# Performance work log

Hardware: AMD Instinct MI355X
Metric: run time of the kernel (lower is better)

The kernel has to match this reference:

```python
import jax, jax.numpy as jnp
import numpy as np

SCALE = 0.02  # init scale for weight matrices


def setup_inputs() -> dict:
    B, M, H = 2048, 64, 1024
    key = jax.random.key(0)
    ks = jax.random.split(key, 10)
    inp = {
        "pose_embed": jax.random.normal(ks[0], (B, H), jnp.float32),
        "query_embed": jax.random.normal(ks[1], (B, H), jnp.float32),
        "h": jax.random.normal(ks[2], (B, H), jnp.float32),
        "c": jax.random.normal(ks[3], (B, H), jnp.float32),
        "memory": jax.random.normal(ks[4], (B, M, H), jnp.float32),
        "W_ih": jax.random.normal(ks[5], (4 * H, H), jnp.float32) * SCALE,
        "W_hh": jax.random.normal(ks[6], (4 * H, H), jnp.float32) * SCALE,
        "b_ih": jnp.zeros((4 * H,), jnp.float32),
        "b_hh": jnp.zeros((4 * H,), jnp.float32),
        "Wq": jax.random.normal(ks[7], (H, H), jnp.float32) * SCALE,
        "bq": jnp.zeros((H,), jnp.float32),
        "Wk": jax.random.normal(ks[8], (H, H), jnp.float32) * SCALE,
        "bk": jnp.zeros((H,), jnp.float32),
        "Wv": jax.random.normal(ks[9], (H, H), jnp.float32) * SCALE,
        "bv": jnp.zeros((H,), jnp.float32),
    }
    return inp


def reference(pose_embed, query_embed, h, c, memory,
              W_ih, W_hh, b_ih, b_hh, Wq, bq, Wk, bk, Wv, bv):
    H = pose_embed.shape[-1]
    # --- LSTMCell step (torch gate order: i, f, g, o) ---
    gates = pose_embed @ W_ih.T + b_ih + h @ W_hh.T + b_hh  # [B, 4H]
    i_g, f_g, g_g, o_g = jnp.split(gates, 4, axis=-1)
    c_new = jax.nn.sigmoid(f_g) * c + jax.nn.sigmoid(i_g) * jnp.tanh(g_g)
    h_new = jax.nn.sigmoid(o_g) * jnp.tanh(c_new)
    # --- FIFO memory update (detach, pop oldest, append new h) ---
    mem = jnp.concatenate(
        [memory[:, 1:], jax.lax.stop_gradient(h_new)[:, None]], axis=1)  # [B, M, H]
    # --- single-query attention over memory ---
    Q = query_embed @ Wq.T + bq                       # [B, H]
    K = mem @ Wk.T + bk                               # [B, M, H]
    V = mem @ Wv.T + bv                               # [B, M, H]
    scores = jnp.einsum('bh,bmh->bm', Q, K) / jnp.sqrt(jnp.float32(H))
    attn = jax.nn.softmax(scores, axis=-1)            # [B, M]
    attended = jnp.einsum('bm,bmh->bh', attn, V)      # [B, H]
    return attended, h_new, c_new
```

## Files before the change

### kernel.cpp

```cpp
#include <hip/hip_runtime.h>
#include <stdint.h>

typedef __attribute__((ext_vector_type(8))) short short8;
typedef __attribute__((ext_vector_type(4))) float f32x4;
typedef unsigned short u16;

#define SBAR() do { __builtin_amdgcn_sched_barrier(0); \
                    __builtin_amdgcn_s_barrier(); \
                    __builtin_amdgcn_sched_barrier(0); } while (0)

__device__ __forceinline__ u16 f2bf(float f) {
  union { float f; uint32_t u; } v; v.f = f;
  return (u16)((v.u + 0x7FFFu + ((v.u >> 16) & 1u)) >> 16);
}
__device__ __forceinline__ float bf2f(u16 u) {
  union { uint32_t u; float f; } v; v.u = (uint32_t)u << 16; return v.f;
}

__device__ __forceinline__ void gl_lds16(const void* g, void* l) {
  __builtin_amdgcn_global_load_lds(
      (const __attribute__((address_space(1))) void*)g,
      (__attribute__((address_space(3))) void*)l, 16, 0, 0);
}

__global__ __launch_bounds__(256) void gemm_bt(
    const u16* __restrict__ A, const u16* __restrict__ B,
    float* __restrict__ Cf, u16* __restrict__ Cb,
    const float* __restrict__ bias1,
    int M, int N, int K)
{
  __shared__ __align__(16) u16 As[128 * 32];
  __shared__ __align__(16) u16 Bs[128 * 32];
  const int t = threadIdx.x;
  const int lane = t & 63;
  const int w = t >> 6;
  const int wr = w >> 1, wc = w & 1;
  const int m0 = blockIdx.y * 128, n0 = blockIdx.x * 128;
  const int lr = lane & 15;
  const int lk = (lane >> 4) * 8;
  const int srow = t >> 2;
  const int scol = (t & 3) * 8;

  const u16* gA = A + (size_t)(m0 + srow) * K + scol;
  const u16* gB = B + (size_t)(n0 + srow) * K + scol;

  f32x4 acc[4][4] = {};

  for (int k0 = 0; k0 < K; k0 += 32) {
    gl_lds16(gA,                  As + t * 8);
    gl_lds16(gA + (size_t)64 * K, As + 2048 + t * 8);
    gl_lds16(gB,                  Bs + t * 8);
    gl_lds16(gB + (size_t)64 * K, Bs + 2048 + t * 8);
    gA += 32; gB += 32;
    __syncthreads();

    short8 a[4], b[4];
#pragma unroll
    for (int m = 0; m < 4; ++m)
      a[m] = *(const short8*)(As + (wr * 64 + m * 16 + lr) * 32 + lk);
#pragma unroll
    for (int n = 0; n < 4; ++n)
      b[n] = *(const short8*)(Bs + (wc * 64 + n * 16 + lr) * 32 + lk);
#pragma unroll
    for (int m = 0; m < 4; ++m)
#pragma unroll
      for (int n = 0; n < 4; ++n)
        acc[m][n] = __builtin_amdgcn_mfma_f32_16x16x32_bf16(a[m], b[n], acc[m][n], 0, 0, 0);
    __syncthreads();
  }

#pragma unroll
  for (int n = 0; n < 4; ++n) {
    int col = n0 + wc * 64 + n * 16 + lr;
    float bsum = bias1 ? bias1[col] : 0.f;
#pragma unroll
    for (int m = 0; m < 4; ++m) {
#pragma unroll
      for (int r = 0; r < 4; ++r) {
        int row = m0 + wr * 64 + m * 16 + (lane >> 4) * 4 + r;
        float vv = acc[m][n][r] + bsum;
        if (Cf) Cf[(size_t)row * N + col] = vv;
        if (Cb) Cb[(size_t)row * N + col] = f2bf(vv);
      }
    }
  }
}

__global__ __launch_bounds__(512) void gates8_k(
    const u16* __restrict__ Xcat, const u16* __restrict__ Wcat,
    u16* __restrict__ gparts)
{
  __shared__ __align__(16) u16 lds[65536];
  const int t = threadIdx.x;
  const int l = t & 63;
  const int w = t >> 6;
  const int wr = w >> 2, wc = w & 3;
  const int bid = blockIdx.x;
  const int tile = bid >> 1, khalf = bid & 1;
  const int m0 = (tile >> 4) * 256;
  const int n0 = (tile & 15) * 256;
  const int lr = l & 15;
  const int l4 = l >> 4;

  const int sr = l >> 3;
  const int sc = ((l & 7) * 8) ^ ((l >> 5) << 4);

  const u16* Abase = Xcat + (size_t)m0 * 2048 + khalf * 1024 + sc;
  const u16* Bbase = Wcat + (size_t)n0 * 2048 + khalf * 1024 + sc;

  #define STAGE(buf, kt) do {                                                  \
    const int kof_ = (kt) * 64;                                                \
    _Pragma("unroll")                                                          \
    for (int hh = 0; hh < 2; ++hh)                                             \
      _Pragma("unroll")                                                        \
      for (int j = 0; j < 2; ++j) {                                            \
        int row_ = hh * 128 + (w + 8 * j) * 8 + sr;                            \
        char* dA = (char*)lds + (buf) * 65536 + hh * 16384 + (w + 8*j) * 1024 + l * 16; \
        char* dB = dA + 32768;                                                 \
        gl_lds16(Abase + (size_t)row_ * 2048 + kof_, dA);                      \
        gl_lds16(Bbase + (size_t)row_ * 2048 + kof_, dB);                      \
      }                                                                        \
  } while (0)

  auto LDA = [&](int buf, int mf, int s) -> short8 {
    int rr = mf * 16 + lr;
    int cb = (s * 64 + l4 * 16) ^ (((rr >> 2) & 1) << 5);
    return *(const short8*)((const char*)lds + buf * 65536 + wr * 16384 + rr * 128 + cb);
  };
  auto LDB = [&](int buf, int nf, int s) -> short8 {
    int rr = (wc & 1) * 64 + nf * 16 + lr;
    int cb = (s * 64 + l4 * 16) ^ (((rr >> 2) & 1) << 5);
    return *(const short8*)((const char*)lds + buf * 65536 + 32768 + (wc >> 1) * 16384 + rr * 128 + cb);
  };

  f32x4 acc[8][4] = {};

  STAGE(0, 0);
  STAGE(1, 1);
  asm volatile("s_waitcnt vmcnt(8)" ::: "memory");
  SBAR();

  for (int kt = 0; kt < 16; ++kt) {
    const int cur = kt & 1;
    short8 a0[4][2], a1[4][2], b[2][2];
#pragma unroll
    for (int i = 0; i < 4; ++i) { a0[i][0] = LDA(cur, i, 0); a0[i][1] = LDA(cur, i, 1); }
#pragma unroll
    for (int n = 0; n < 2; ++n) { b[n][0] = LDB(cur, n, 0); b[n][1] = LDB(cur, n, 1); }
    __builtin_amdgcn_s_setprio(1);
#pragma unroll
    for (int i = 0; i < 4; ++i)
#pragma unroll
      for (int n = 0; n < 2; ++n)
#pragma unroll
        for (int s = 0; s < 2; ++s)
          acc[i][n] = __builtin_amdgcn_mfma_f32_16x16x32_bf16(a0[i][s], b[n][s], acc[i][n], 0, 0, 0);
    __builtin_amdgcn_s_setprio(0);
#pragma unroll
    for (int i = 0; i < 4; ++i) { a1[i][0] = LDA(cur, 4 + i, 0); a1[i][1] = LDA(cur, 4 + i, 1); }
    __builtin_amdgcn_s_setprio(1);
#pragma unroll
    for (int i = 0; i < 4; ++i)
#pragma unroll
      for (int n = 0; n < 2; ++n)
#pragma unroll
        for (int s = 0; s < 2; ++s)
          acc[4 + i][n] = __builtin_amdgcn_mfma_f32_16x16x32_bf16(a1[i][s], b[n][s], acc[4 + i][n], 0, 0, 0);
    __builtin_amdgcn_s_setprio(0);
#pragma unroll
    for (int n = 0; n < 2; ++n) { b[n][0] = LDB(cur, 2 + n, 0); b[n][1] = LDB(cur, 2 + n, 1); }
    __builtin_amdgcn_s_setprio(1);
#pragma unroll
    for (int i = 0; i < 4; ++i)
#pragma unroll
      for (int n = 0; n < 2; ++n)
#pragma unroll
        for (int s = 0; s < 2; ++s)
          acc[4 + i][2 + n] = __builtin_amdgcn_mfma_f32_16x16x32_bf16(a1[i][s], b[n][s], acc[4 + i][2 + n], 0, 0, 0);
#pragma unroll
    for (int i = 0; i < 4; ++i)
#pragma unroll
      for (int n = 0; n < 2; ++n)
#pragma unroll
        for (int s = 0; s < 2; ++s)
          acc[i][2 + n] = __builtin_amdgcn_mfma_f32_16x16x32_bf16(a0[i][s], b[n][s], acc[i][2 + n], 0, 0, 0);
    __builtin_amdgcn_s_setprio(0);

    SBAR();
    if (kt + 2 < 16) {
      STAGE(cur, kt + 2);
      asm volatile("s_waitcnt vmcnt(8)" ::: "memory");
    } else {
      asm volatile("s_waitcnt vmcnt(0)" ::: "memory");
    }
    SBAR();
  }
  #undef STAGE

  u16* out = gparts + (size_t)khalf * 2048 * 4096;
#pragma unroll
  for (int nf = 0; nf < 4; ++nf) {
    int col = n0 + wc * 64 + nf * 16 + lr;
#pragma unroll
    for (int mf = 0; mf < 8; ++mf)
#pragma unroll
      for (int r = 0; r < 4; ++r) {
        int row = m0 + wr * 128 + mf * 16 + l4 * 4 + r;
        out[(size_t)row * 4096 + col] = f2bf(acc[mf][nf][r]);
      }
  }
}

__global__ __launch_bounds__(256) void attn_k(
    const float* __restrict__ Qk, const float* __restrict__ mem,
    float* __restrict__ attst)
{
  const int t = threadIdx.x;
  const int lane = t & 63;
  const int b = blockIdx.x * 4 + (t >> 6);
  const float* q = Qk + (size_t)b * 1024;
  f32x4 qv[4];
#pragma unroll
  for (int i = 0; i < 4; ++i)
    qv[i] = *(const f32x4*)(q + (i * 64 + lane) * 4);
  const float* mb = mem + (size_t)b * 65536;

  float m_run = -3e38f, l = 0.f;
  f32x4 cx[4] = {};

  for (int qd = 0; qd < 15; ++qd) {
    const float* r0 = mb + (size_t)(1 + qd * 4) * 1024;
    f32x4 rv[4][4];
    float s[4] = {0.f, 0.f, 0.f, 0.f};
#pragma unroll
    for (int rr = 0; rr < 4; ++rr)
#pragma unroll
      for (int i = 0; i < 4; ++i) {
        rv[rr][i] = __builtin_nontemporal_load(
            (const f32x4*)(r0 + rr * 1024 + (i * 64 + lane) * 4));
        s[rr] += rv[rr][i][0] * qv[i][0] + rv[rr][i][1] * qv[i][1] +
                 rv[rr][i][2] * qv[i][2] + rv[rr][i][3] * qv[i][3];
      }
#pragma unroll
    for (int rr = 0; rr < 4; ++rr) {
#pragma unroll
      for (int off = 32; off; off >>= 1) s[rr] += __shfl_xor(s[rr], off);
      s[rr] *= 0.03125f;
    }
#pragma unroll
    for (int rr = 0; rr < 4; ++rr) {
      if (s[rr] <= m_run + 8.f) {
        float e = __expf(s[rr] - m_run);
        l += e;
#pragma unroll
        for (int i = 0; i < 4; ++i) cx[i] += rv[rr][i] * e;
      } else {
        float sc = __expf(m_run - s[rr]);
        m_run = s[rr];
        l = l * sc + 1.f;
#pragma unroll
        for (int i = 0; i < 4; ++i) cx[i] = cx[i] * sc + rv[rr][i];
      }
    }
  }
  for (int r = 61; r <= 63; ++r) {
    const float* row = mb + (size_t)r * 1024;
    f32x4 rv[4];
    float s = 0.f;
#pragma unroll
    for (int i = 0; i < 4; ++i) {
      rv[i] = __builtin_nontemporal_load(
          (const f32x4*)(row + (i * 64 + lane) * 4));
      s += rv[i][0] * qv[i][0] + rv[i][1] * qv[i][1] +
           rv[i][2] * qv[i][2] + rv[i][3] * qv[i][3];
    }
#pragma unroll
    for (int off = 32; off; off >>= 1) s += __shfl_xor(s, off);
    s *= 0.03125f;
    if (s <= m_run + 8.f) {
      float e = __expf(s - m_run);
      l += e;
#pragma unroll
      for (int i = 0; i < 4; ++i) cx[i] += rv[i] * e;
    } else {
      float sc = __expf(m_run - s);
      m_run = s;
      l = l * sc + 1.f;
#pragma unroll
      for (int i = 0; i < 4; ++i) cx[i] = cx[i] * sc + rv[i];
    }
  }
  float* st = attst + (size_t)b * 1032;
#pragma unroll
  for (int i = 0; i < 4; ++i)
    *(f32x4*)(st + (i * 64 + lane) * 4) = cx[i];
  if (lane == 0) { st[1024] = m_run; st[1025] = l; }
}

__global__ __launch_bounds__(256) void prep_k(
    const float* __restrict__ pose, const float* __restrict__ h,
    const float* __restrict__ W_ih, const float* __restrict__ W_hh,
    const float* __restrict__ query, const float* __restrict__ Wv,
    const float* __restrict__ Wq, const float* __restrict__ Wk,
    u16* __restrict__ xcat, u16* __restrict__ wcat,
    u16* __restrict__ qry, u16* __restrict__ wvb,
    u16* __restrict__ wqtb, u16* __restrict__ wktb)
{
  __shared__ u16 tile[64][65];
  int blk = blockIdx.x;
  int t = threadIdx.x;
  if (blk >= 15360) {
    const float* src; u16* dst; int tblk;
    if (blk < 15616) { src = Wq; dst = wqtb; tblk = blk - 15360; }
    else             { src = Wk; dst = wktb; tblk = blk - 15616; }
    int tr = (tblk >> 4) * 64, tc = (tblk & 15) * 64;
    int tx = t & 63;
    int ty = (t >> 6) * 16;
#pragma unroll
    for (int i = 0; i < 16; ++i)
      tile[ty + i][tx] = f2bf(src[(size_t)(tr + ty + i) * 1024 + tc + tx]);
    __syncthreads();
#pragma unroll
    for (int i = 0; i < 16; ++i)
      dst[(size_t)(tc + ty + i) * 1024 + tr + tx] = tile[tx][ty + i];
    return;
  }
  const float* src; u16* dst; int ostride, ooff, base;
  if (blk < 2048)       { src = pose;  dst = xcat; ostride = 2048; ooff = 0;    base = 0; }
  else if (blk < 4096)  { src = h;     dst = xcat; ostride = 2048; ooff = 1024; base = 2048; }
  else if (blk < 8192)  { src = W_ih;  dst = wcat; ostride = 2048; ooff = 0;    base = 4096; }
  else if (blk < 12288) { src = W_hh;  dst = wcat; ostride = 2048; ooff = 1024; base = 8192; }
  else if (blk < 14336) { src = query; dst = qry;  ostride = 1024; ooff = 0;    base = 12288; }
  else                  { src = Wv;    dst = wvb;  ostride = 1024; ooff = 0;    base = 14336; }
  int r = blk - base;
  int cc = t * 4;
  float4 v = *(const float4*)(src + (size_t)r * 1024 + cc);
  ushort4 o; o.x = f2bf(v.x); o.y = f2bf(v.y); o.z = f2bf(v.z); o.w = f2bf(v.w);
  *(ushort4*)(dst + (size_t)r * ostride + ooff + cc) = o;
}

__global__ __launch_bounds__(256) void bqwk_k(
    const float* __restrict__ bq, const float* __restrict__ Wk,
    float* __restrict__ qkb)
{
  int n = blockIdx.x * 256 + threadIdx.x;
  int j0 = blockIdx.y * 64;
  float s = 0.f;
#pragma unroll 8
  for (int j = j0; j < j0 + 64; ++j) s += bq[j] * Wk[(size_t)j * 1024 + n];
  atomicAdd(&qkb[n], s);
}

__global__ __launch_bounds__(256) void lstmfin_k(
    const u16* __restrict__ gparts, const float* __restrict__ c,
    const float* __restrict__ b_ih, const float* __restrict__ b_hh,
    const float* __restrict__ Qk, const float* __restrict__ attst,
    float* __restrict__ out_h, float* __restrict__ out_c,
    u16* __restrict__ ctxb)
{
  const int b = blockIdx.x;
  const int t = threadIdx.x;
  const int lane = t & 63, wv_id = t >> 6;
  const int p = t * 4;
  const u16* g0 = gparts + (size_t)b * 4096;
  const u16* g1 = g0 + (size_t)2048 * 4096;
  float4 cv = *(const float4*)(c + (size_t)b * 1024 + p);
  float cvs[4] = {cv.x, cv.y, cv.z, cv.w};

  float hn[4], cn[4];
  float gsum[4][4];
#pragma unroll
  for (int gi = 0; gi < 4; ++gi) {
    ushort4 a = *(const ushort4*)(g0 + gi * 1024 + p);
    ushort4 bb = *(const ushort4*)(g1 + gi * 1024 + p);
    float4 bi = *(const float4*)(b_ih + gi * 1024 + p);
    float4 bh = *(const float4*)(b_hh + gi * 1024 + p);
    gsum[gi][0] = bf2f(a.x) + bf2f(bb.x) + bi.x + bh.x;
    gsum[gi][1] = bf2f(a.y) + bf2f(bb.y) + bi.y + bh.y;
    gsum[gi][2] = bf2f(a.z) + bf2f(bb.z) + bi.z + bh.z;
    gsum[gi][3] = bf2f(a.w) + bf2f(bb.w) + bi.w + bh.w;
  }
#pragma unroll
  for (int j = 0; j < 4; ++j) {
    float si = 1.f / (1.f + __expf(-gsum[0][j]));
    float sf = 1.f / (1.f + __expf(-gsum[1][j]));
    float so = 1.f / (1.f + __expf(-gsum[3][j]));
    float tg = 2.f / (1.f + __expf(-2.f * gsum[2][j])) - 1.f;
    cn[j] = sf * cvs[j] + si * tg;
    float tc2 = 2.f / (1.f + __expf(-2.f * cn[j])) - 1.f;
    hn[j] = so * tc2;
  }
  *(float4*)(out_c + (size_t)b * 1024 + p) = make_float4(cn[0], cn[1], cn[2], cn[3]);
  *(float4*)(out_h + (size_t)b * 1024 + p) = make_float4(hn[0], hn[1], hn[2], hn[3]);

  float4 qv = *(const float4*)(Qk + (size_t)b * 1024 + p);
  float part = qv.x * hn[0] + qv.y * hn[1] + qv.z * hn[2] + qv.w * hn[3];
#pragma unroll
  for (int off = 32; off; off >>= 1) part += __shfl_xor(part, off);
  __shared__ float red[4];
  if (lane == 0) red[wv_id] = part;
  __syncthreads();
  float s_last = (red[0] + red[1] + red[2] + red[3]) * 0.03125f;

  const float* st = attst + (size_t)b * 1032;
  float m_run = st[1024], l = st[1025];
  float4 cx = *(const float4*)(st + p);
  if (s_last <= m_run + 8.f) {
    float e = __expf(s_last - m_run);
    l += e;
    cx.x += e * hn[0]; cx.y += e * hn[1]; cx.z += e * hn[2]; cx.w += e * hn[3];
  } else {
    float sc = __expf(m_run - s_last);
    l = l * sc + 1.f;
    cx.x = cx.x * sc + hn[0]; cx.y = cx.y * sc + hn[1];
    cx.z = cx.z * sc + hn[2]; cx.w = cx.w * sc + hn[3];
  }
  float inv = 1.f / l;
  ushort4 o;
  o.x = f2bf(cx.x * inv); o.y = f2bf(cx.y * inv);
  o.z = f2bf(cx.z * inv); o.w = f2bf(cx.w * inv);
  *(ushort4*)(ctxb + (size_t)b * 1024 + p) = o;
}

extern "C" void kernel_launch(void* const* d_in, const int* in_sizes, int n_in,
                              void* d_out, int out_size, void* d_ws, size_t ws_size,
                              hipStream_t stream) {
  const int Bb = 2048, Hh = 1024;
  const float* pose  = (const float*)d_in[0];
  const float* query = (const float*)d_in[1];
  const float* h     = (const float*)d_in[2];
  const float* c     = (const float*)d_in[3];
  const float* mem   = (const float*)d_in[4];
  const float* W_ih  = (const float*)d_in[5];
  const float* W_hh  = (const float*)d_in[6];
  const float* b_ih  = (const float*)d_in[7];
  const float* b_hh  = (const float*)d_in[8];
  const float* Wq    = (const float*)d_in[9];
  const float* bq    = (const float*)d_in[10];
  const float* Wk    = (const float*)d_in[11];
  const float* Wv    = (const float*)d_in[13];
  const float* bv    = (const float*)d_in[14];

  float* out_att = (float*)d_out;
  float* out_h   = out_att + (size_t)Bb * Hh;
  float* out_c   = out_h + (size_t)Bb * Hh;

  char* wp = (char*)d_ws;
  auto alloc = [&](size_t bytes) {
    char* p = wp; wp += (bytes + 255) & ~(size_t)255; return p;
  };
  u16*   Xcat  = (u16*)alloc((size_t)2048 * 2048 * 2);
  u16*   Wcat  = (u16*)alloc((size_t)4096 * 2048 * 2);
  u16*   Qryb  = (u16*)alloc((size_t)2048 * 1024 * 2);
  u16*   WqTb  = (u16*)alloc((size_t)1024 * 1024 * 2);
  u16*   WkTb  = (u16*)alloc((size_t)1024 * 1024 * 2);
  u16*   Gb    = (u16*)alloc((size_t)1024 * 1024 * 2);
  u16*   Wvb   = (u16*)alloc((size_t)1024 * 1024 * 2);
  u16*   gparts= (u16*)alloc((size_t)2 * 2048 * 4096 * 2);
  float* qkb   = (float*)alloc((size_t)1024 * 4);
  float* Qk    = (float*)alloc((size_t)2048 * 1024 * 4);
  u16*   ctxb  = (u16*)alloc((size_t)2048 * 1024 * 2);
  float* attst = (float*)Qryb;

  prep_k<<<15872, 256, 0, stream>>>(pose, h, W_ih, W_hh, query, Wv, Wq, Wk,
                                    Xcat, Wcat, Qryb, Wvb, WqTb, WkTb);

  hipMemsetAsync(qkb, 0, 1024 * sizeof(float), stream);
  bqwk_k<<<dim3(4, 16), 256, 0, stream>>>(bq, Wk, qkb);

  gemm_bt<<<dim3(8, 8), 256, 0, stream>>>(
      WkTb, WqTb, nullptr, Gb, nullptr, 1024, 1024, 1024);

  gemm_bt<<<dim3(8, 16), 256, 0, stream>>>(
      Qryb, Gb, Qk, nullptr, qkb, 2048, 1024, 1024);

  gates8_k<<<256, 512, 0, stream>>>(Xcat, Wcat, gparts);

  attn_k<<<512, 256, 0, stream>>>(Qk, mem, attst);

  lstmfin_k<<<2048, 256, 0, stream>>>(gparts, c, b_ih, b_hh, Qk, attst,
                                      out_h, out_c, ctxb);

  gemm_bt<<<dim3(8, 16), 256, 0, stream>>>(
      ctxb, Wvb, out_att, nullptr, bv, 2048, 1024, 1024);
}
```

Before: 248.4 us.

## Split prep kernel and overlap Wk^T·Wq GEMM with bulk bf16 conversion

Replaces the single prep kernel, the memset, the bias-projection kernel and the small Wk^T·Wq GEMM with two launches. The first converts query and transposes Wq/Wk. The second runs the 1024x1024 G GEMM and the bq·Wk reduction in its first blocks while the remaining blocks do the large fp32-to-bf16 conversions of pose, h, W_ih, W_hh and Wv. The aim is to cut launch count and to hide the small GEMM, which uses too few blocks to fill the device, behind bandwidth-bound conversion work. The in-kernel GEMM is a simple unpipelined MFMA loop, and the bias reduction is serial over 1024 rows per thread, so these blocks may finish last and become the tail.

```diff
diff --git a/kernel.cpp b/kernel.cpp
--- a/kernel.cpp
+++ b/kernel.cpp
@@ -211,6 +211,119 @@
   }
 }
 
+__global__ __launch_bounds__(256) void prepQ_k(
+    const float* __restrict__ query, const float* __restrict__ Wq,
+    const float* __restrict__ Wk,
+    u16* __restrict__ qry, u16* __restrict__ wqtb, u16* __restrict__ wktb)
+{
+  __shared__ u16 tile[64][65];
+  int blk = blockIdx.x;
+  int t = threadIdx.x;
+  if (blk < 2048) {
+    int cc = t * 4;
+    float4 v = *(const float4*)(query + (size_t)blk * 1024 + cc);
+    ushort4 o; o.x = f2bf(v.x); o.y = f2bf(v.y); o.z = f2bf(v.z); o.w = f2bf(v.w);
+    *(ushort4*)(qry + (size_t)blk * 1024 + cc) = o;
+    return;
+  }
+  const float* src; u16* dst; int tblk;
+  if (blk < 2304) { src = Wq; dst = wqtb; tblk = blk - 2048; }
+  else            { src = Wk; dst = wktb; tblk = blk - 2304; }
+  int tr = (tblk >> 4) * 64, tc = (tblk & 15) * 64;
+  int tx = t & 63;
+  int ty = (t >> 6) * 16;
+#pragma unroll
+  for (int i = 0; i < 16; ++i)
+    tile[ty + i][tx] = f2bf(src[(size_t)(tr + ty + i) * 1024 + tc + tx]);
+  __syncthreads();
+#pragma unroll
+  for (int i = 0; i < 16; ++i)
+    dst[(size_t)(tc + ty + i) * 1024 + tr + tx] = tile[tx][ty + i];
+}
+
+__global__ __launch_bounds__(256) void prepRG_k(
+    const float* __restrict__ pose, const float* __restrict__ h,
+    const float* __restrict__ W_ih, const float* __restrict__ W_hh,
+    const float* __restrict__ Wv,
+    const u16* __restrict__ WkTb, const u16* __restrict__ WqTb,
+    const float* __restrict__ bq, const float* __restrict__ Wk,
+    u16* __restrict__ xcat, u16* __restrict__ wcat, u16* __restrict__ wvb,
+    u16* __restrict__ Gb, float* __restrict__ qkb)
+{
+  __shared__ __align__(16) u16 As[128 * 32];
+  __shared__ __align__(16) u16 Bs[128 * 32];
+  const int blk = blockIdx.x;
+  const int t = threadIdx.x;
+  if (blk < 64) {
+    const int lane = t & 63;
+    const int w = t >> 6;
+    const int wr = w >> 1, wc = w & 1;
+    const int m0 = (blk >> 3) * 128, n0 = (blk & 7) * 128;
+    const int lr = lane & 15;
+    const int lk = (lane >> 4) * 8;
+    const int srow = t >> 2;
+    const int scol = (t & 3) * 8;
+    const u16* gA = WkTb + (size_t)(m0 + srow) * 1024 + scol;
+    const u16* gB = WqTb + (size_t)(n0 + srow) * 1024 + scol;
+    f32x4 acc[4][4] = {};
+    for (int k0 = 0; k0 < 1024; k0 += 32) {
+      gl_lds16(gA,                     As + t * 8);
+      gl_lds16(gA + (size_t)64 * 1024, As + 2048 + t * 8);
+      gl_lds16(gB,                     Bs + t * 8);
+      gl_lds16(gB + (size_t)64 * 1024, Bs + 2048 + t * 8);
+      gA += 32; gB += 32;
+      __syncthreads();
+      short8 a[4], b[4];
+#pragma unroll
+      for (int m = 0; m < 4; ++m)
+        a[m] = *(const short8*)(As + (wr * 64 + m * 16 + lr) * 32 + lk);
+#pragma unroll
+      for (int n = 0; n < 4; ++n)
+        b[n] = *(const short8*)(Bs + (wc * 64 + n * 16 + lr) * 32 + lk);
+#pragma unroll
+      for (int m = 0; m < 4; ++m)
+#pragma unroll
+        for (int n = 0; n < 4; ++n)
+          acc[m][n] = __builtin_amdgcn_mfma_f32_16x16x32_bf16(a[m], b[n], acc[m][n], 0, 0, 0);
+      __syncthreads();
+    }
+#pragma unroll
+    for (int n = 0; n < 4; ++n) {
+      int col = n0 + wc * 64 + n * 16 + lr;
+#pragma unroll
+      for (int m = 0; m < 4; ++m)
+#pragma unroll
+        for (int r = 0; r < 4; ++r) {
+          int row = m0 + wr * 64 + m * 16 + (lane >> 4) * 4 + r;
+          Gb[(size_t)row * 1024 + col] = f2bf(acc[m][n][r]);
+        }
+    }
+    return;
+  }
+  if (blk < 68) {
+    int n = (blk - 64) * 256 + t;
+    float s0 = 0.f, s1 = 0.f;
+    for (int j = 0; j < 1024; j += 2) {
+      s0 += bq[j]     * Wk[(size_t)j * 1024 + n];
+      s1 += bq[j + 1] * Wk[(size_t)(j + 1) * 1024 + n];
+    }
+    qkb[n] = s0 + s1;
+    return;
+  }
+  int b2 = blk - 68;
+  const float* src; u16* dst; int ostride, ooff, base;
+  if (b2 < 2048)       { src = pose;  dst = xcat; ostride = 2048; ooff = 0;    base = 0; }
+  else if (b2 < 4096)  { src = h;     dst = xcat; ostride = 2048; ooff = 1024; base = 2048; }
+  else if (b2 < 8192)  { src = W_ih;  dst = wcat; ostride = 2048; ooff = 0;    base = 4096; }
+  else if (b2 < 12288) { src = W_hh;  dst = wcat; ostride = 2048; ooff = 1024; base = 8192; }
+  else                 { src = Wv;    dst = wvb;  ostride = 1024; ooff = 0;    base = 12288; }
+  int r = b2 - base;
+  int cc = t * 4;
+  float4 v = *(const float4*)(src + (size_t)r * 1024 + cc);
+  ushort4 o; o.x = f2bf(v.x); o.y = f2bf(v.y); o.z = f2bf(v.z); o.w = f2bf(v.w);
+  *(ushort4*)(dst + (size_t)r * ostride + ooff + cc) = o;
+}
+
 __global__ __launch_bounds__(256) void attn_k(
     const float* __restrict__ Qk, const float* __restrict__ mem,
     float* __restrict__ attst)
@@ -295,60 +408,6 @@
   for (int i = 0; i < 4; ++i)
     *(f32x4*)(st + (i * 64 + lane) * 4) = cx[i];
   if (lane == 0) { st[1024] = m_run; st[1025] = l; }
-}
-
-__global__ __launch_bounds__(256) void prep_k(
-    const float* __restrict__ pose, const float* __restrict__ h,
-    const float* __restrict__ W_ih, const float* __restrict__ W_hh,
-    const float* __restrict__ query, const float* __restrict__ Wv,
-    const float* __restrict__ Wq, const float* __restrict__ Wk,
-    u16* __restrict__ xcat, u16* __restrict__ wcat,
-    u16* __restrict__ qry, u16* __restrict__ wvb,
-    u16* __restrict__ wqtb, u16* __restrict__ wktb)
-{
-  __shared__ u16 tile[64][65];
-  int blk = blockIdx.x;
-  int t = threadIdx.x;
-  if (blk >= 15360) {
-    const float* src; u16* dst; int tblk;
-    if (blk < 15616) { src = Wq; dst = wqtb; tblk = blk - 15360; }
-    else             { src = Wk; dst = wktb; tblk = blk - 15616; }
-    int tr = (tblk >> 4) * 64, tc = (tblk & 15) * 64;
-    int tx = t & 63;
-    int ty = (t >> 6) * 16;
-#pragma unroll
-    for (int i = 0; i < 16; ++i)
-      tile[ty + i][tx] = f2bf(src[(size_t)(tr + ty + i) * 1024 + tc + tx]);
-    __syncthreads();
-#pragma unroll
-    for (int i = 0; i < 16; ++i)
-      dst[(size_t)(tc + ty + i) * 1024 + tr + tx] = tile[tx][ty + i];
-    return;
-  }
-  const float* src; u16* dst; int ostride, ooff, base;
-  if (blk < 2048)       { src = pose;  dst = xcat; ostride = 2048; ooff = 0;    base = 0; }
-  else if (blk < 4096)  { src = h;     dst = xcat; ostride = 2048; ooff = 1024; base = 2048; }
-  else if (blk < 8192)  { src = W_ih;  dst = wcat; ostride = 2048; ooff = 0;    base = 4096; }
-  else if (blk < 12288) { src = W_hh;  dst = wcat; ostride = 2048; ooff = 1024; base = 8192; }
-  else if (blk < 14336) { src = query; dst = qry;  ostride = 1024; ooff = 0;    base = 12288; }
-  else                  { src = Wv;    dst = wvb;  ostride = 1024; ooff = 0;    base = 14336; }
-  int r = blk - base;
-  int cc = t * 4;
-  float4 v = *(const float4*)(src + (size_t)r * 1024 + cc);
-  ushort4 o; o.x = f2bf(v.x); o.y = f2bf(v.y); o.z = f2bf(v.z); o.w = f2bf(v.w);
-  *(ushort4*)(dst + (size_t)r * ostride + ooff + cc) = o;
-}
-
-__global__ __launch_bounds__(256) void bqwk_k(
-    const float* __restrict__ bq, const float* __restrict__ Wk,
-    float* __restrict__ qkb)
-{
-  int n = blockIdx.x * 256 + threadIdx.x;
-  int j0 = blockIdx.y * 64;
-  float s = 0.f;
-#pragma unroll 8
-  for (int j = j0; j < j0 + 64; ++j) s += bq[j] * Wk[(size_t)j * 1024 + n];
-  atomicAdd(&qkb[n], s);
 }
 
 __global__ __launch_bounds__(256) void lstmfin_k(
@@ -462,14 +521,11 @@
   u16*   ctxb  = (u16*)alloc((size_t)2048 * 1024 * 2);
   float* attst = (float*)Qryb;
 
-  prep_k<<<15872, 256, 0, stream>>>(pose, h, W_ih, W_hh, query, Wv, Wq, Wk,
-                                    Xcat, Wcat, Qryb, Wvb, WqTb, WkTb);
-
-  hipMemsetAsync(qkb, 0, 1024 * sizeof(float), stream);
-  bqwk_k<<<dim3(4, 16), 256, 0, stream>>>(bq, Wk, qkb);
-
-  gemm_bt<<<dim3(8, 8), 256, 0, stream>>>(
-      WkTb, WqTb, nullptr, Gb, nullptr, 1024, 1024, 1024);
+  prepQ_k<<<2560, 256, 0, stream>>>(query, Wq, Wk, Qryb, WqTb, WkTb);
+
+  prepRG_k<<<13380, 256, 0, stream>>>(pose, h, W_ih, W_hh, Wv,
+                                      WkTb, WqTb, bq, Wk,
+                                      Xcat, Wcat, Wvb, Gb, qkb);
 
   gemm_bt<<<dim3(8, 16), 256, 0, stream>>>(
       Qryb, Gb, Qk, nullptr, qkb, 2048, 1024, 1024);
```

Result: faster. 241.1 us (-3.0%).
